# Kernel tuning notes

Hardware: AMD Instinct MI355X
Metric: run time of the kernel (lower is better)

## Reference

```python
import jax, jax.numpy as jnp
import numpy as np

N_NODES = 100000
N_EDGES = 1600000
D_IN = 256
HEADS = 8
D_HEAD = 32  # out_channels // heads = 256 // 8
NEG_SLOPE = 0.2
BN_EPS = 1e-5


def setup_inputs() -> dict:
    key = jax.random.key(0)
    ks = jax.random.split(key, 8)
    x = jax.random.normal(ks[0], (N_NODES, D_IN), dtype=jnp.float32)
    edge_index = jax.random.randint(ks[1], (2, N_EDGES), 0, N_NODES, dtype=jnp.int32)
    # GATConv parameters (concat=True): lin weight, attention vectors, bias
    W = jax.random.normal(ks[2], (D_IN, HEADS * D_HEAD), dtype=jnp.float32) / np.sqrt(D_IN)
    att_src = jax.random.normal(ks[3], (HEADS, D_HEAD), dtype=jnp.float32) / np.sqrt(D_HEAD)
    att_dst = jax.random.normal(ks[4], (HEADS, D_HEAD), dtype=jnp.float32) / np.sqrt(D_HEAD)
    bias = jax.random.normal(ks[5], (HEADS * D_HEAD,), dtype=jnp.float32) * 0.01
    gamma = jnp.ones((HEADS * D_HEAD,), dtype=jnp.float32)
    beta = jnp.zeros((HEADS * D_HEAD,), dtype=jnp.float32)
    return {"x": x, "edge_index": edge_index, "W": W, "att_src": att_src,
            "att_dst": att_dst, "bias": bias, "gamma": gamma, "beta": beta}


def reference(x, edge_index, W, att_src, att_dst, bias, gamma, beta):
    N = x.shape[0]
    H, D = att_src.shape
    # per-head linear projection: [N, H, D]
    xh = (x @ W).reshape(N, H, D)
    a_src = jnp.einsum('nhd,hd->nh', xh, att_src)  # [N, H]
    a_dst = jnp.einsum('nhd,hd->nh', xh, att_dst)  # [N, H]
    # add self loops (GATConv default add_self_loops=True)
    loops = jnp.arange(N, dtype=edge_index.dtype)
    src = jnp.concatenate([edge_index[0], loops])  # message sources j
    dst = jnp.concatenate([edge_index[1], loops])  # aggregation targets i
    # attention logits per edge, LeakyReLU(0.2)
    e = jax.nn.leaky_relu(a_src[src] + a_dst[dst], NEG_SLOPE)  # [E+N, H]
    # scatter-softmax over edges grouped by destination node
    m = jax.ops.segment_max(e, dst, num_segments=N)
    e = jnp.exp(e - m[dst])
    denom = jax.ops.segment_sum(e, dst, num_segments=N)
    alpha = e / denom[dst]  # [E+N, H]
    # weighted message scatter-add
    msg = xh[src] * alpha[:, :, None]  # [E+N, H, D]
    out = jax.ops.segment_sum(msg, dst, num_segments=N).reshape(N, H * D) + bias
    # BatchNorm1d over nodes (batch statistics, deterministic)
    mean = jnp.mean(out, axis=0)
    var = jnp.var(out, axis=0)
    out = (out - mean) * jax.lax.rsqrt(var + BN_EPS) * gamma + beta
    # residual (in_channels == out_channels)
    return out + x
```

## Files before the change

kernel.cpp:

```cpp
#include <hip/hip_runtime.h>
#include <hip/hip_bf16.h>
#include <math.h>


#define N_NODES 100000
#define N_EDGES 1600000
#define NEG_SLOPE 0.2f
#define BN_EPS  1e-5f

typedef __attribute__((ext_vector_type(8))) short short8;
typedef __attribute__((ext_vector_type(4))) float f32x4;

#define OFF_XHB     0
#define OFF_ASRC    51200000
#define OFF_ADST    54400000
#define OFF_ROWPTR  57600000
#define OFF_CURSOR  58000256
#define OFF_COUNTS  58400512
#define OFF_CSRSRC  58800768
#define OFF_ACCUM   65200768
#define OFF_BSUMS   65202816
#define OFF_BOFF    65203328
#define OFF_WT      65203968
#define OFF_PART    65335040

__device__ __forceinline__ float leaky(float v) {
    return v > 0.f ? v : NEG_SLOPE * v;
}
__device__ __forceinline__ unsigned short f2bf(float f) {
    unsigned int u = __float_as_uint(f);
    unsigned int r = (u + 0x7fffu + ((u >> 16) & 1u)) >> 16;
    return (unsigned short)r;
}
__device__ __forceinline__ float bf2f(unsigned short u) {
    return __uint_as_float(((unsigned int)u) << 16);
}

__global__ __launch_bounds__(256) void castW(const float* __restrict__ W,
                                             unsigned short* __restrict__ Wt) {
    const int k = blockIdx.x;
    const int n = threadIdx.x;
    Wt[n * 256 + k] = f2bf(W[k * 256 + n]);
}

__global__ __launch_bounds__(256) void gemm_mfma(const float* __restrict__ A,
                                                 const unsigned short* __restrict__ Wt,
                                                 unsigned short* __restrict__ xhb) {
    __shared__ unsigned short Asl[2][128 * 40];
    __shared__ unsigned short Bsl[2][256 * 40];
    const int tid = threadIdx.x;
    const int wid = tid >> 6, lane = tid & 63;
    const int wr = wid >> 1, wc = wid & 1;
    const int row0 = blockIdx.x * 128;

    f32x4 acc[4][8];
#pragma unroll
    for (int m = 0; m < 4; ++m)
#pragma unroll
        for (int n = 0; n < 8; ++n) acc[m][n] = (f32x4){0.f, 0.f, 0.f, 0.f};

    float4 areg[4];
    int4 breg[4];

#pragma unroll
    for (int q = 0; q < 4; ++q) {
        const int lin = tid + q * 256;
        const int r = lin >> 3, c4 = (lin & 7) * 4;
        const int row = row0 + r;
        areg[q] = (row < N_NODES) ? *(const float4*)&A[(size_t)row * 256 + c4]
                                  : make_float4(0.f, 0.f, 0.f, 0.f);
    }
    {
        const int4* src = (const int4*)&Wt[tid * 256 + 0];
        breg[0] = src[0]; breg[1] = src[1]; breg[2] = src[2]; breg[3] = src[3];
    }
#pragma unroll
    for (int q = 0; q < 4; ++q) {
        const int lin = tid + q * 256;
        const int r = lin >> 3, c4 = (lin & 7) * 4;
        unsigned short* d = &Asl[0][r * 40 + c4];
        d[0] = f2bf(areg[q].x); d[1] = f2bf(areg[q].y);
        d[2] = f2bf(areg[q].z); d[3] = f2bf(areg[q].w);
    }
    {
        int4* d = (int4*)&Bsl[0][tid * 40];
        d[0] = breg[0]; d[1] = breg[1]; d[2] = breg[2]; d[3] = breg[3];
    }
    __syncthreads();

    const int r16 = lane & 15;
    const int k8 = (lane >> 4) * 8;

    int buf = 0;
    for (int ks = 0; ks < 8; ++ks) {
        const bool more = ks < 7;
        if (more) {
            const int kk = (ks + 1) * 32;
#pragma unroll
            for (int q = 0; q < 4; ++q) {
                const int lin = tid + q * 256;
                const int r = lin >> 3, c4 = (lin & 7) * 4;
                const int row = row0 + r;
                areg[q] = (row < N_NODES)
                              ? *(const float4*)&A[(size_t)row * 256 + kk + c4]
                              : make_float4(0.f, 0.f, 0.f, 0.f);
            }
            const int4* src = (const int4*)&Wt[tid * 256 + kk];
            breg[0] = src[0]; breg[1] = src[1]; breg[2] = src[2]; breg[3] = src[3];
        }
        short8 afr[4], bfr[8];
#pragma unroll
        for (int m = 0; m < 4; ++m)
            afr[m] = *(const short8*)&Asl[buf][(wr * 64 + m * 16 + r16) * 40 + k8];
#pragma unroll
        for (int n = 0; n < 8; ++n)
            bfr[n] = *(const short8*)&Bsl[buf][(wc * 128 + n * 16 + r16) * 40 + k8];
#pragma unroll
        for (int m = 0; m < 4; ++m)
#pragma unroll
            for (int n = 0; n < 8; ++n)
                acc[m][n] = __builtin_amdgcn_mfma_f32_16x16x32_bf16(
                    afr[m], bfr[n], acc[m][n], 0, 0, 0);
        if (more) {
            const int nb = buf ^ 1;
#pragma unroll
            for (int q = 0; q < 4; ++q) {
                const int lin = tid + q * 256;
                const int r = lin >> 3, c4 = (lin & 7) * 4;
                unsigned short* d = &Asl[nb][r * 40 + c4];
                d[0] = f2bf(areg[q].x); d[1] = f2bf(areg[q].y);
                d[2] = f2bf(areg[q].z); d[3] = f2bf(areg[q].w);
            }
            int4* d = (int4*)&Bsl[nb][tid * 40];
            d[0] = breg[0]; d[1] = breg[1]; d[2] = breg[2]; d[3] = breg[3];
            __syncthreads();
            buf = nb;
        }
    }

#pragma unroll
    for (int m = 0; m < 4; ++m) {
        const int rbase = row0 + wr * 64 + m * 16 + (lane >> 4) * 4;
#pragma unroll
        for (int n = 0; n < 8; ++n) {
            const int col = wc * 128 + n * 16 + r16;
#pragma unroll
            for (int reg = 0; reg < 4; ++reg) {
                const int row = rbase + reg;
                if (row < N_NODES)
                    xhb[(size_t)row * 256 + col] = f2bf(acc[m][n][reg]);
            }
        }
    }
}

__global__ __launch_bounds__(256) void att_vec(const unsigned short* __restrict__ xhb,
                                               const float* __restrict__ att_src,
                                               const float* __restrict__ att_dst,
                                               float* __restrict__ a_src,
                                               float* __restrict__ a_dst) {
    const int wid = (blockIdx.x * blockDim.x + threadIdx.x) >> 6;
    const int lane = threadIdx.x & 63;
    if (wid >= N_NODES) return;
    const ushort4 xv4 = *(const ushort4*)&xhb[(size_t)wid * 256 + lane * 4];
    const float x0 = bf2f(xv4.x), x1 = bf2f(xv4.y), x2 = bf2f(xv4.z), x3 = bf2f(xv4.w);
    const int h = lane >> 3;
    const int doff = (lane & 7) * 4;
    const float4 sv = *(const float4*)&att_src[h * 32 + doff];
    const float4 dv = *(const float4*)&att_dst[h * 32 + doff];
    float ss = x0 * sv.x + x1 * sv.y + x2 * sv.z + x3 * sv.w;
    float sd = x0 * dv.x + x1 * dv.y + x2 * dv.z + x3 * dv.w;
#pragma unroll
    for (int m = 1; m < 8; m <<= 1) {
        ss += __shfl_xor(ss, m);
        sd += __shfl_xor(sd, m);
    }
    if ((lane & 7) == 0) {
        a_src[wid * 8 + h] = ss;
        a_dst[wid * 8 + h] = sd;
    }
}

__global__ void count_edges(const int* __restrict__ ei, int* __restrict__ counts) {
    const int e = blockIdx.x * blockDim.x + threadIdx.x;
    if (e < N_EDGES) atomicAdd(&counts[ei[N_EDGES + e]], 1);
}

__global__ __launch_bounds__(1024) void scan1(const int* __restrict__ counts,
                                              int* __restrict__ row_ptr,
                                              int* __restrict__ bsums) {
    __shared__ int s[1024];
    const int tid = threadIdx.x;
    const int idx = blockIdx.x * 1024 + tid;
    const int v = (idx < N_NODES) ? counts[idx] : 0;
    s[tid] = v;
    __syncthreads();
#pragma unroll
    for (int off = 1; off < 1024; off <<= 1) {
        const int add = (tid >= off) ? s[tid - off] : 0;
        __syncthreads();
        s[tid] += add;
        __syncthreads();
    }
    if (idx < N_NODES) row_ptr[idx] = s[tid] - v;
    if (tid == 1023) bsums[blockIdx.x] = s[1023];
}

__global__ __launch_bounds__(128) void scan2(const int* __restrict__ bsums,
                                             int* __restrict__ boff, int nb) {
    __shared__ int s[128];
    const int tid = threadIdx.x;
    const int v = (tid < nb) ? bsums[tid] : 0;
    s[tid] = v;
    __syncthreads();
#pragma unroll
    for (int off = 1; off < 128; off <<= 1) {
        const int add = (tid >= off) ? s[tid - off] : 0;
        __syncthreads();
        s[tid] += add;
        __syncthreads();
    }
    if (tid < nb) boff[tid] = s[tid] - v;
}

__global__ __launch_bounds__(1024) void scan3(int* __restrict__ row_ptr,
                                              int* __restrict__ cursor,
                                              const int* __restrict__ boff) {
    const int idx = blockIdx.x * 1024 + threadIdx.x;
    if (idx < N_NODES) {
        const int r = row_ptr[idx] + boff[blockIdx.x];
        row_ptr[idx] = r;
        cursor[idx] = r;
    }
    if (idx == 0) row_ptr[N_NODES] = N_EDGES;
}

__global__ void fill_csr(const int* __restrict__ ei, int* __restrict__ cursor,
                         int* __restrict__ csr_src) {
    const int e = blockIdx.x * blockDim.x + threadIdx.x;
    if (e < N_EDGES) {
        const int s = ei[e];
        const int d = ei[N_EDGES + e];
        const int pos = atomicAdd(&cursor[d], 1);
        csr_src[pos] = s;
    }
}

__global__ __launch_bounds__(256) void aggregate(const unsigned short* __restrict__ xhb,
                                                 const float* __restrict__ a_src,
                                                 const float* __restrict__ a_dst,
                                                 const int* __restrict__ row_ptr,
                                                 const int* __restrict__ csr_src,
                                                 const float* __restrict__ bias,
                                                 float* __restrict__ outbuf) {
    __shared__ int   j_cache[4][64];
    __shared__ float w_cache[4][64 * 8];
    const int wv = threadIdx.x >> 6;
    const int lane = threadIdx.x & 63;
    const int i = blockIdx.x * 4 + wv;
    const int beg = row_ptr[i], end = row_ptr[i + 1];
    const int deg = end - beg;
    const int deg64 = deg < 64 ? deg : 64;

    const int h1 = lane & 7, sub = lane >> 3;
    const float ad1 = a_dst[i * 8 + h1];
    float sm_p = (sub == 0) ? __expf(leaky(a_src[i * 8 + h1] + ad1)) : 0.f;
    for (int t = sub; t < deg64; t += 8) {
        const int j = csr_src[beg + t];
        if (h1 == 0) j_cache[wv][t] = j;
        const float w = __expf(leaky(a_src[j * 8 + h1] + ad1));
        w_cache[wv][t * 8 + h1] = w;
        sm_p += w;
    }
#pragma unroll
    for (int m = 8; m < 64; m <<= 1) sm_p += __shfl_xor(sm_p, m);
    __syncthreads();

    const int h2 = lane >> 3;
    float sm = __shfl(sm_p, h2);
    const float ad2 = a_dst[i * 8 + h2];
    const float as2 = a_src[i * 8 + h2];
    const float wself = __expf(leaky(as2 + ad2));
    const ushort4 sv4 = *(const ushort4*)&xhb[(size_t)i * 256 + lane * 4];
    float4 acc;
    acc.x = wself * bf2f(sv4.x); acc.y = wself * bf2f(sv4.y);
    acc.z = wself * bf2f(sv4.z); acc.w = wself * bf2f(sv4.w);

#pragma unroll 4
    for (int t = 0; t < deg64; ++t) {
        const int j = j_cache[wv][t];
        const float w = w_cache[wv][t * 8 + h2];
        const ushort4 v4 = *(const ushort4*)&xhb[(size_t)j * 256 + lane * 4];
        acc.x = fmaf(w, bf2f(v4.x), acc.x);
        acc.y = fmaf(w, bf2f(v4.y), acc.y);
        acc.z = fmaf(w, bf2f(v4.z), acc.z);
        acc.w = fmaf(w, bf2f(v4.w), acc.w);
    }
    for (int t = 64; t < deg; ++t) {
        const int j = csr_src[beg + t];
        const float w = __expf(leaky(a_src[j * 8 + h2] + ad2));
        sm += w;
        const ushort4 v4 = *(const ushort4*)&xhb[(size_t)j * 256 + lane * 4];
        acc.x = fmaf(w, bf2f(v4.x), acc.x);
        acc.y = fmaf(w, bf2f(v4.y), acc.y);
        acc.z = fmaf(w, bf2f(v4.z), acc.z);
        acc.w = fmaf(w, bf2f(v4.w), acc.w);
    }
    const float inv = 1.0f / sm;
    const float4 bv = *(const float4*)&bias[lane * 4];
    acc.x = acc.x * inv + bv.x;
    acc.y = acc.y * inv + bv.y;
    acc.z = acc.z * inv + bv.z;
    acc.w = acc.w * inv + bv.w;
    *(float4*)&outbuf[(size_t)i * 256 + lane * 4] = acc;
}

__global__ __launch_bounds__(256) void bn_stats1(const float* __restrict__ outbuf,
                                                 float* __restrict__ part) {
    const int c = threadIdx.x;
    float s = 0.f, s2 = 0.f;
    for (int r = blockIdx.x; r < N_NODES; r += 2048) {
        const float v = outbuf[(size_t)r * 256 + c];
        s += v; s2 += v * v;
    }
    part[(size_t)blockIdx.x * 512 + c] = s;
    part[(size_t)blockIdx.x * 512 + 256 + c] = s2;
}

__global__ __launch_bounds__(512) void bn_stats2(const float* __restrict__ part,
                                                 float* __restrict__ accum) {
    const int c = threadIdx.x;
    float s = 0.f;
    for (int b = blockIdx.x; b < 2048; b += 64)
        s += part[(size_t)b * 512 + c];
    atomicAdd(&accum[c], s);
}

__global__ __launch_bounds__(256) void bn_final(float* __restrict__ out,
                                                const float* __restrict__ x,
                                                const float* __restrict__ accum,
                                                const float* __restrict__ gamma,
                                                const float* __restrict__ beta) {
    const size_t total4 = (size_t)N_NODES * 64;
    const size_t stride = (size_t)gridDim.x * blockDim.x;
    const float invN = 1.0f / (float)N_NODES;
    for (size_t f = blockIdx.x * blockDim.x + threadIdx.x; f < total4; f += stride) {
        const int c4 = ((int)(f & 63)) * 4;
        float4 v = *(float4*)&out[f * 4];
        const float4 xv = *(const float4*)&x[f * 4];
        const float4 sv = *(const float4*)&accum[c4];
        const float4 qv = *(const float4*)&accum[256 + c4];
        const float4 gv = *(const float4*)&gamma[c4];
        const float4 bv = *(const float4*)&beta[c4];
        float mean, var;
        mean = sv.x * invN; var = qv.x * invN - mean * mean;
        v.x = (v.x - mean) * rsqrtf(var + BN_EPS) * gv.x + bv.x + xv.x;
        mean = sv.y * invN; var = qv.y * invN - mean * mean;
        v.y = (v.y - mean) * rsqrtf(var + BN_EPS) * gv.y + bv.y + xv.y;
        mean = sv.z * invN; var = qv.z * invN - mean * mean;
        v.z = (v.z - mean) * rsqrtf(var + BN_EPS) * gv.z + bv.z + xv.z;
        mean = sv.w * invN; var = qv.w * invN - mean * mean;
        v.w = (v.w - mean) * rsqrtf(var + BN_EPS) * gv.w + bv.w + xv.w;
        *(float4*)&out[f * 4] = v;
    }
}

extern "C" void kernel_launch(void* const* d_in, const int* in_sizes, int n_in,
                              void* d_out, int out_size, void* d_ws, size_t ws_size,
                              hipStream_t stream) {
    const float* x       = (const float*)d_in[0];
    const int*   ei      = (const int*)d_in[1];
    const float* W       = (const float*)d_in[2];
    const float* att_src = (const float*)d_in[3];
    const float* att_dst = (const float*)d_in[4];
    const float* bias    = (const float*)d_in[5];
    const float* gamma   = (const float*)d_in[6];
    const float* beta    = (const float*)d_in[7];
    float* out = (float*)d_out;

    char* ws = (char*)d_ws;
    unsigned short* xhb = (unsigned short*)(ws + OFF_XHB);
    float* a_src   = (float*)(ws + OFF_ASRC);
    float* a_dst   = (float*)(ws + OFF_ADST);
    int*   row_ptr = (int*)(ws + OFF_ROWPTR);
    int*   cursor  = (int*)(ws + OFF_CURSOR);
    int*   counts  = (int*)(ws + OFF_COUNTS);
    int*   csr_src = (int*)(ws + OFF_CSRSRC);
    float* accum   = (float*)(ws + OFF_ACCUM);
    int*   bsums   = (int*)(ws + OFF_BSUMS);
    int*   boff    = (int*)(ws + OFF_BOFF);
    unsigned short* Wt = (unsigned short*)(ws + OFF_WT);
    float* part    = (float*)(ws + OFF_PART);

    hipMemsetAsync(counts, 0, N_NODES * sizeof(int), stream);
    hipMemsetAsync(accum, 0, 512 * sizeof(float), stream);

    castW<<<256, 256, 0, stream>>>(W, Wt);
    gemm_mfma<<<(N_NODES + 127) / 128, 256, 0, stream>>>(x, Wt, xhb);

    att_vec<<<(N_NODES * 64 + 255) / 256, 256, 0, stream>>>(xhb, att_src, att_dst,
                                                            a_src, a_dst);

    const int nsb = (N_NODES + 1023) / 1024;
    count_edges<<<(N_EDGES + 255) / 256, 256, 0, stream>>>(ei, counts);
    scan1<<<nsb, 1024, 0, stream>>>(counts, row_ptr, bsums);
    scan2<<<1, 128, 0, stream>>>(bsums, boff, nsb);
    scan3<<<nsb, 1024, 0, stream>>>(row_ptr, cursor, boff);
    fill_csr<<<(N_EDGES + 255) / 256, 256, 0, stream>>>(ei, cursor, csr_src);

    aggregate<<<N_NODES / 4, 256, 0, stream>>>(
        xhb, a_src, a_dst, row_ptr, csr_src, bias, out);

    bn_stats1<<<2048, 256, 0, stream>>>(out, part);
    bn_stats2<<<64, 512, 0, stream>>>(part, accum);
    bn_final<<<2048, 256, 0, stream>>>(out, x, accum, gamma, beta);
}
```

Baseline: 649.8 us.

## Pre-cast x to bf16 and split GEMM into 128x128 column tiles; add nontemporal stores

Adds a separate kernel that casts x to bf16 in workspace, and the GEMM then loads bf16 tiles directly with 16-byte copies instead of converting fp32 inside the main loop. The GEMM grid gains a second dimension so each block computes a 128x128 output tile. This halves the accumulator registers and LDS per block and doubles the block count, at the cost of reading the A tile twice. Nontemporal loads and stores are also used for the aggregate output and the final BN pass to reduce cache pollution. The trade-off is an extra pass over x (an fp32 read plus a bf16 write) and a larger workspace.

Measured after the change: 673.5 us. +3.7%, slower.

```diff
diff --git a/kernel.cpp b/kernel.cpp
--- a/kernel.cpp
+++ b/kernel.cpp
@@ -12,17 +12,18 @@
 typedef __attribute__((ext_vector_type(4))) float f32x4;
 
 #define OFF_XHB     0
-#define OFF_ASRC    51200000
-#define OFF_ADST    54400000
-#define OFF_ROWPTR  57600000
-#define OFF_CURSOR  58000256
-#define OFF_COUNTS  58400512
-#define OFF_CSRSRC  58800768
-#define OFF_ACCUM   65200768
-#define OFF_BSUMS   65202816
-#define OFF_BOFF    65203328
-#define OFF_WT      65203968
-#define OFF_PART    65335040
+#define OFF_XB      51200000
+#define OFF_ASRC    102400000
+#define OFF_ADST    105600000
+#define OFF_ROWPTR  108800000
+#define OFF_CURSOR  109200256
+#define OFF_COUNTS  109600512
+#define OFF_CSRSRC  110000768
+#define OFF_ACCUM   116400768
+#define OFF_BSUMS   116402816
+#define OFF_BOFF    116403328
+#define OFF_WT      116403968
+#define OFF_PART    116535040
 
 __device__ __forceinline__ float leaky(float v) {
     return v > 0.f ? v : NEG_SLOPE * v;
@@ -34,6 +35,18 @@
 }
 __device__ __forceinline__ float bf2f(unsigned short u) {
     return __uint_as_float(((unsigned int)u) << 16);
+}
+
+__global__ __launch_bounds__(256) void cast_x(const float* __restrict__ x,
+                                              unsigned short* __restrict__ xb) {
+    const size_t t = (size_t)blockIdx.x * 256 + threadIdx.x;
+    const float4 a = *(const float4*)&x[t * 8];
+    const float4 b = *(const float4*)&x[t * 8 + 4];
+    ushort4 lo, hi;
+    lo.x = f2bf(a.x); lo.y = f2bf(a.y); lo.z = f2bf(a.z); lo.w = f2bf(a.w);
+    hi.x = f2bf(b.x); hi.y = f2bf(b.y); hi.z = f2bf(b.z); hi.w = f2bf(b.w);
+    *(ushort4*)&xb[t * 8] = lo;
+    *(ushort4*)&xb[t * 8 + 4] = hi;
 }
 
 __global__ __launch_bounds__(256) void castW(const float* __restrict__ W,
@@ -43,48 +56,38 @@
     Wt[n * 256 + k] = f2bf(W[k * 256 + n]);
 }
 
-__global__ __launch_bounds__(256) void gemm_mfma(const float* __restrict__ A,
+__global__ __launch_bounds__(256) void gemm_mfma(const unsigned short* __restrict__ xb,
                                                  const unsigned short* __restrict__ Wt,
                                                  unsigned short* __restrict__ xhb) {
     __shared__ unsigned short Asl[2][128 * 40];
-    __shared__ unsigned short Bsl[2][256 * 40];
+    __shared__ unsigned short Bsl[2][128 * 40];
     const int tid = threadIdx.x;
     const int wid = tid >> 6, lane = tid & 63;
     const int wr = wid >> 1, wc = wid & 1;
     const int row0 = blockIdx.x * 128;
-
-    f32x4 acc[4][8];
+    const int col0 = blockIdx.y * 128;
+
+    f32x4 acc[4][4];
 #pragma unroll
     for (int m = 0; m < 4; ++m)
 #pragma unroll
-        for (int n = 0; n < 8; ++n) acc[m][n] = (f32x4){0.f, 0.f, 0.f, 0.f};
-
-    float4 areg[4];
-    int4 breg[4];
-
-#pragma unroll
-    for (int q = 0; q < 4; ++q) {
-        const int lin = tid + q * 256;
-        const int r = lin >> 3, c4 = (lin & 7) * 4;
-        const int row = row0 + r;
-        areg[q] = (row < N_NODES) ? *(const float4*)&A[(size_t)row * 256 + c4]
-                                  : make_float4(0.f, 0.f, 0.f, 0.f);
-    }
-    {
-        const int4* src = (const int4*)&Wt[tid * 256 + 0];
-        breg[0] = src[0]; breg[1] = src[1]; breg[2] = src[2]; breg[3] = src[3];
-    }
-#pragma unroll
-    for (int q = 0; q < 4; ++q) {
-        const int lin = tid + q * 256;
-        const int r = lin >> 3, c4 = (lin & 7) * 4;
-        unsigned short* d = &Asl[0][r * 40 + c4];
-        d[0] = f2bf(areg[q].x); d[1] = f2bf(areg[q].y);
-        d[2] = f2bf(areg[q].z); d[3] = f2bf(areg[q].w);
-    }
-    {
-        int4* d = (int4*)&Bsl[0][tid * 40];
-        d[0] = breg[0]; d[1] = breg[1]; d[2] = breg[2]; d[3] = breg[3];
+        for (int n = 0; n < 4; ++n) acc[m][n] = (f32x4){0.f, 0.f, 0.f, 0.f};
+
+    int4 areg[2], breg[2];
+    const int r_a[2] = {(tid + 0) >> 2, (tid + 256) >> 2};
+    const int kq[2] = {(tid & 3) * 8, (tid & 3) * 8};
+
+#pragma unroll
+    for (int q = 0; q < 2; ++q) {
+        const int row = row0 + r_a[q];
+        areg[q] = (row < N_NODES) ? *(const int4*)&xb[(size_t)row * 256 + kq[q]]
+                                  : make_int4(0, 0, 0, 0);
+        breg[q] = *(const int4*)&Wt[(size_t)(col0 + r_a[q]) * 256 + kq[q]];
+    }
+#pragma unroll
+    for (int q = 0; q < 2; ++q) {
+        *(int4*)&Asl[0][r_a[q] * 40 + kq[q]] = areg[q];
+        *(int4*)&Bsl[0][r_a[q] * 40 + kq[q]] = breg[q];
     }
     __syncthreads();
 
@@ -97,42 +100,34 @@
         if (more) {
             const int kk = (ks + 1) * 32;
 #pragma unroll
-            for (int q = 0; q < 4; ++q) {
-                const int lin = tid + q * 256;
-                const int r = lin >> 3, c4 = (lin & 7) * 4;
-                const int row = row0 + r;
+            for (int q = 0; q < 2; ++q) {
+                const int row = row0 + r_a[q];
                 areg[q] = (row < N_NODES)
-                              ? *(const float4*)&A[(size_t)row * 256 + kk + c4]
-                              : make_float4(0.f, 0.f, 0.f, 0.f);
+                              ? *(const int4*)&xb[(size_t)row * 256 + kk + kq[q]]
+                              : make_int4(0, 0, 0, 0);
+                breg[q] = *(const int4*)&Wt[(size_t)(col0 + r_a[q]) * 256 + kk + kq[q]];
             }
-            const int4* src = (const int4*)&Wt[tid * 256 + kk];
-            breg[0] = src[0]; breg[1] = src[1]; breg[2] = src[2]; breg[3] = src[3];
         }
-        short8 afr[4], bfr[8];
+        short8 afr[4], bfr[4];
 #pragma unroll
         for (int m = 0; m < 4; ++m)
             afr[m] = *(const short8*)&Asl[buf][(wr * 64 + m * 16 + r16) * 40 + k8];
 #pragma unroll
-        for (int n = 0; n < 8; ++n)
-            bfr[n] = *(const short8*)&Bsl[buf][(wc * 128 + n * 16 + r16) * 40 + k8];
+        for (int n = 0; n < 4; ++n)
+            bfr[n] = *(const short8*)&Bsl[buf][(wc * 64 + n * 16 + r16) * 40 + k8];
 #pragma unroll
         for (int m = 0; m < 4; ++m)
 #pragma unroll
-            for (int n = 0; n < 8; ++n)
+            for (int n = 0; n < 4; ++n)
                 acc[m][n] = __builtin_amdgcn_mfma_f32_16x16x32_bf16(
                     afr[m], bfr[n], acc[m][n], 0, 0, 0);
         if (more) {
             const int nb = buf ^ 1;
 #pragma unroll
-            for (int q = 0; q < 4; ++q) {
-                const int lin = tid + q * 256;
-                const int r = lin >> 3, c4 = (lin & 7) * 4;
-                unsigned short* d = &Asl[nb][r * 40 + c4];
-                d[0] = f2bf(areg[q].x); d[1] = f2bf(areg[q].y);
-                d[2] = f2bf(areg[q].z); d[3] = f2bf(areg[q].w);
+            for (int q = 0; q < 2; ++q) {
+                *(int4*)&Asl[nb][r_a[q] * 40 + kq[q]] = areg[q];
+                *(int4*)&Bsl[nb][r_a[q] * 40 + kq[q]] = breg[q];
             }
-            int4* d = (int4*)&Bsl[nb][tid * 40];
-            d[0] = breg[0]; d[1] = breg[1]; d[2] = breg[2]; d[3] = breg[3];
             __syncthreads();
             buf = nb;
         }
@@ -142,8 +137,8 @@
     for (int m = 0; m < 4; ++m) {
         const int rbase = row0 + wr * 64 + m * 16 + (lane >> 4) * 4;
 #pragma unroll
-        for (int n = 0; n < 8; ++n) {
-            const int col = wc * 128 + n * 16 + r16;
+        for (int n = 0; n < 4; ++n) {
+            const int col = col0 + wc * 64 + n * 16 + r16;
 #pragma unroll
             for (int reg = 0; reg < 4; ++reg) {
                 const int row = rbase + reg;
@@ -308,11 +303,12 @@
     }
     const float inv = 1.0f / sm;
     const float4 bv = *(const float4*)&bias[lane * 4];
-    acc.x = acc.x * inv + bv.x;
-    acc.y = acc.y * inv + bv.y;
-    acc.z = acc.z * inv + bv.z;
-    acc.w = acc.w * inv + bv.w;
-    *(float4*)&outbuf[(size_t)i * 256 + lane * 4] = acc;
+    f32x4 res;
+    res[0] = acc.x * inv + bv.x;
+    res[1] = acc.y * inv + bv.y;
+    res[2] = acc.z * inv + bv.z;
+    res[3] = acc.w * inv + bv.w;
+    __builtin_nontemporal_store(res, (f32x4*)&outbuf[(size_t)i * 256 + lane * 4]);
 }
 
 __global__ __launch_bounds__(256) void bn_stats1(const float* __restrict__ outbuf,
@@ -347,21 +343,22 @@
     for (size_t f = blockIdx.x * blockDim.x + threadIdx.x; f < total4; f += stride) {
         const int c4 = ((int)(f & 63)) * 4;
         float4 v = *(float4*)&out[f * 4];
-        const float4 xv = *(const float4*)&x[f * 4];
+        const f32x4 xv = __builtin_nontemporal_load((const f32x4*)&x[f * 4]);
         const float4 sv = *(const float4*)&accum[c4];
         const float4 qv = *(const float4*)&accum[256 + c4];
         const float4 gv = *(const float4*)&gamma[c4];
         const float4 bv = *(const float4*)&beta[c4];
+        f32x4 r;
         float mean, var;
         mean = sv.x * invN; var = qv.x * invN - mean * mean;
-        v.x = (v.x - mean) * rsqrtf(var + BN_EPS) * gv.x + bv.x + xv.x;
+        r[0] = (v.x - mean) * rsqrtf(var + BN_EPS) * gv.x + bv.x + xv[0];
         mean = sv.y * invN; var = qv.y * invN - mean * mean;
-        v.y = (v.y - mean) * rsqrtf(var + BN_EPS) * gv.y + bv.y + xv.y;
+        r[1] = (v.y - mean) * rsqrtf(var + BN_EPS) * gv.y + bv.y + xv[1];
         mean = sv.z * invN; var = qv.z * invN - mean * mean;
-        v.z = (v.z - mean) * rsqrtf(var + BN_EPS) * gv.z + bv.z + xv.z;
+        r[2] = (v.z - mean) * rsqrtf(var + BN_EPS) * gv.z + bv.z + xv[2];
         mean = sv.w * invN; var = qv.w * invN - mean * mean;
-        v.w = (v.w - mean) * rsqrtf(var + BN_EPS) * gv.w + bv.w + xv.w;
-        *(float4*)&out[f * 4] = v;
+        r[3] = (v.w - mean) * rsqrtf(var + BN_EPS) * gv.w + bv.w + xv[3];
+        __builtin_nontemporal_store(r, (f32x4*)&out[f * 4]);
     }
 }
 
@@ -380,6 +377,7 @@
 
     char* ws = (char*)d_ws;
     unsigned short* xhb = (unsigned short*)(ws + OFF_XHB);
+    unsigned short* xb  = (unsigned short*)(ws + OFF_XB);
     float* a_src   = (float*)(ws + OFF_ASRC);
     float* a_dst   = (float*)(ws + OFF_ADST);
     int*   row_ptr = (int*)(ws + OFF_ROWPTR);
@@ -395,8 +393,9 @@
     hipMemsetAsync(counts, 0, N_NODES * sizeof(int), stream);
     hipMemsetAsync(accum, 0, 512 * sizeof(float), stream);
 
+    cast_x<<<12500, 256, 0, stream>>>(x, xb);
     castW<<<256, 256, 0, stream>>>(W, Wt);
-    gemm_mfma<<<(N_NODES + 127) / 128, 256, 0, stream>>>(x, Wt, xhb);
+    gemm_mfma<<<dim3((N_NODES + 127) / 128, 2), 256, 0, stream>>>(xb, Wt, xhb);
 
     att_vec<<<(N_NODES * 64 + 255) / 256, 256, 0, stream>>>(xhb, att_src, att_dst,
                                                             a_src, a_dst);
```
